# Kernel optimization log

Hardware: AMD Instinct MI355X
Metric: run time of the kernel (lower is better)

Reference implementation:

```python
import jax, jax.numpy as jnp
import numpy as np

B, T, U, D, V = 4, 400, 100, 512, 1024


def setup_inputs() -> dict:
    key = jax.random.key(0)
    k1, k2, k3, k4, k5, k6 = jax.random.split(key, 6)
    return {
        "source_encodings": jax.random.normal(k1, (B, T, D), dtype=jnp.float32),
        "source_lengths": jax.random.randint(k2, (B,), 1, T + 1, dtype=jnp.int32),
        "target_encodings": jax.random.normal(k3, (B, U, D), dtype=jnp.float32),
        "target_lengths": jax.random.randint(k4, (B,), 1, U + 1, dtype=jnp.int32),
        "W": jax.random.normal(k5, (V, D), dtype=jnp.float32) * (1.0 / np.sqrt(D)),
        "b": jax.random.normal(k6, (V,), dtype=jnp.float32) * 0.01,
    }


def reference(source_encodings, source_lengths, target_encodings, target_lengths, W, b):
    # broadcast add: (B,T,1,D) + (B,1,U,D) -> (B,T,U,D)
    joint = source_encodings[:, :, None, :] + target_encodings[:, None, :, :]
    tanh_out = jnp.tanh(joint)
    # linear: (B,T,U,D) @ (D,V) + b -> (B,T,U,V)
    output = jnp.einsum("btud,vd->btuv", tanh_out, W) + b
    return output, source_lengths, target_lengths
```

## Files before the change

### kernel.cpp

```cpp
#include <hip/hip_runtime.h>

#define Bb 4
#define Tt 400
#define Uu 100
#define Dd 512
#define Vv 1024
#define Mtot (Bb * Tt * Uu)
#define OUT_ELEMS ((size_t)Mtot * Vv)
#define NT 8

typedef unsigned short u16;
typedef unsigned int u32;
typedef short bf16x8 __attribute__((ext_vector_type(8)));
typedef float f32x4 __attribute__((ext_vector_type(4)));
typedef u16 u16x4 __attribute__((ext_vector_type(4)));

__device__ __forceinline__ u16 f2bf(float x) {
    union { float f; u32 u; } v; v.f = x;
    u32 r = v.u + 0x7FFFu + ((v.u >> 16) & 1u);
    return (u16)(r >> 16);
}

__device__ __forceinline__ void async16(const void* g, void* l) {
    __builtin_amdgcn_global_load_lds(
        (const __attribute__((address_space(1))) u32*)g,
        (__attribute__((address_space(3))) u32*)l,
        16, 0, 0);
}

__global__ void tanh_fuse(const float* __restrict__ src,
                          const float* __restrict__ tgt,
                          u16* __restrict__ A) {
    int idx = blockIdx.x * 256 + threadIdx.x;
    int d4 = idx & 127;
    int m  = idx >> 7;
    int b  = m / 40000;
    int r  = m - b * 40000;
    int t  = r / 100;
    int u  = r - t * 100;
    const float4 s = ((const float4*)src)[(b * Tt + t) * 128 + d4];
    const float4 g = ((const float4*)tgt)[(b * Uu + u) * 128 + d4];
    u16x4 o;
    o.x = f2bf(tanhf(s.x + g.x));
    o.y = f2bf(tanhf(s.y + g.y));
    o.z = f2bf(tanhf(s.z + g.z));
    o.w = f2bf(tanhf(s.w + g.w));
    ((u16x4*)A)[idx] = o;
}

__global__ void wconv(const float* __restrict__ W, u16* __restrict__ Wb,
                      const int* __restrict__ slen, const int* __restrict__ tlen,
                      float* __restrict__ out) {
    int idx = blockIdx.x * 256 + threadIdx.x;
    float4 w = ((const float4*)W)[idx];
    u16x4 o;
    o.x = f2bf(w.x); o.y = f2bf(w.y); o.z = f2bf(w.z); o.w = f2bf(w.w);
    ((u16x4*)Wb)[idx] = o;
    if (idx < 4)      out[OUT_ELEMS + idx] = (float)slen[idx];
    else if (idx < 8) out[OUT_ELEMS + idx] = (float)tlen[idx - 4];
}


__device__ __forceinline__ void stg2(const u16* g, u16* l, int off0, int loff) {
    async16(g + off0,         l + loff);
    async16(g + off0 + 32768, l + loff + 4096);
}

__global__ __launch_bounds__(512, 2) void gemm8(const u16* __restrict__ A,
                                                const u16* __restrict__ Wb,
                                                const float* __restrict__ bias,
                                                float* __restrict__ out) {
    __shared__ u16 sm[65536];

    const int tid = threadIdx.x;
    const int orig = blockIdx.x;
    const int xcd = orig & 7, loc = orig >> 3;
    const int wg = (xcd < 4 ? xcd * 313 : 1252 + (xcd - 4) * 312) + loc;
    const int bm = wg >> 2;
    const int bn = wg & 3;

    const int lane = tid & 63, wave = tid >> 6;
    const int wm = wave >> 2, wn = wave & 3;
    const int l15 = lane & 15, quad = lane >> 4;
    const int sx = l15 & 7;
    const int c0 = (quad ^ sx) * 8;
    const int c1 = ((4 | quad) ^ sx) * 8;

    const int srow = tid >> 3;
    const int skc  = (tid & 7) ^ (srow & 7);
    const int off0 = srow * 512 + skc * 8;
    const int loff = tid * 8;

    const u16* GA = A  + (size_t)bm * 131072;
    const u16* GB = Wb + (size_t)bn * 131072;

    f32x4 acc[8][4] = {};

    stg2(GA,                 sm,                 off0, loff);
    stg2(GA + 65536,         sm + 8192,          off0, loff);
    stg2(GB,                 sm + 16384,         off0, loff);
    stg2(GB + 65536,         sm + 16384 + 8192,  off0, loff);
    stg2(GA + 64,            sm + 32768,         off0, loff);
    asm volatile("s_waitcnt vmcnt(2)" ::: "memory");
    __builtin_amdgcn_s_barrier();
    __builtin_amdgcn_sched_barrier(0);

    const int bhalf = wn >> 1;
    const int bsub  = (wn & 1) * 4096;

    for (int S = 0; S < NT; ++S) {
        const u16* pA = sm + (S & 1) * 32768 + wm * 8192 + l15 * 64;
        const u16* pB = sm + (S & 1) * 32768 + 16384 + bhalf * 8192 + bsub + l15 * 64;
        u16* nb = sm + ((S + 1) & 1) * 32768;
        u16* cb = sm + (S & 1) * 32768;
        bf16x8 af[4][2], bA[2][2], bB[2][2];

#pragma unroll
        for (int i = 0; i < 4; ++i) {
            af[i][0] = *(const bf16x8*)&pA[i * 1024 + c0];
            af[i][1] = *(const bf16x8*)&pA[i * 1024 + c1];
        }
#pragma unroll
        for (int j = 0; j < 2; ++j) {
            bA[j][0] = *(const bf16x8*)&pB[j * 1024 + c0];
            bA[j][1] = *(const bf16x8*)&pB[j * 1024 + c1];
        }
        if (S + 1 < NT) stg2(GA + 65536 + (S + 1) * 64, nb + 8192, off0, loff);
        __builtin_amdgcn_s_barrier();
        asm volatile("s_waitcnt lgkmcnt(0)" ::: "memory");
        __builtin_amdgcn_sched_barrier(0);
        __builtin_amdgcn_s_setprio(1);
#pragma unroll
        for (int i = 0; i < 4; ++i)
#pragma unroll
            for (int j = 0; j < 2; ++j)
#pragma unroll
                for (int kk = 0; kk < 2; ++kk)
                    acc[i][j] = __builtin_amdgcn_mfma_f32_16x16x32_bf16(
                        af[i][kk], bA[j][kk], acc[i][j], 0, 0, 0);
        __builtin_amdgcn_s_setprio(0);
        __builtin_amdgcn_s_barrier();
        asm volatile("" ::: "memory");

#pragma unroll
        for (int j = 0; j < 2; ++j) {
            bB[j][0] = *(const bf16x8*)&pB[(j + 2) * 1024 + c0];
            bB[j][1] = *(const bf16x8*)&pB[(j + 2) * 1024 + c1];
        }
        if (S + 1 < NT) stg2(GB + (S + 1) * 64, nb + 16384, off0, loff);
        __builtin_amdgcn_s_barrier();
        asm volatile("s_waitcnt lgkmcnt(0)" ::: "memory");
        __builtin_amdgcn_sched_barrier(0);
        __builtin_amdgcn_s_setprio(1);
#pragma unroll
        for (int i = 0; i < 4; ++i)
#pragma unroll
            for (int j = 0; j < 2; ++j)
#pragma unroll
                for (int kk = 0; kk < 2; ++kk)
                    acc[i][j + 2] = __builtin_amdgcn_mfma_f32_16x16x32_bf16(
                        af[i][kk], bB[j][kk], acc[i][j + 2], 0, 0, 0);
        __builtin_amdgcn_s_setprio(0);
        __builtin_amdgcn_s_barrier();
        asm volatile("" ::: "memory");

#pragma unroll
        for (int i = 0; i < 4; ++i) {
            af[i][0] = *(const bf16x8*)&pA[(i + 4) * 1024 + c0];
            af[i][1] = *(const bf16x8*)&pA[(i + 4) * 1024 + c1];
        }
        if (S + 1 < NT) stg2(GB + 65536 + (S + 1) * 64, nb + 16384 + 8192, off0, loff);
        __builtin_amdgcn_s_barrier();
        asm volatile("s_waitcnt lgkmcnt(0)" ::: "memory");
        __builtin_amdgcn_sched_barrier(0);
        __builtin_amdgcn_s_setprio(1);
#pragma unroll
        for (int i = 0; i < 4; ++i)
#pragma unroll
            for (int j = 0; j < 2; ++j)
#pragma unroll
                for (int kk = 0; kk < 2; ++kk)
                    acc[i + 4][j + 2] = __builtin_amdgcn_mfma_f32_16x16x32_bf16(
                        af[i][kk], bB[j][kk], acc[i + 4][j + 2], 0, 0, 0);
        __builtin_amdgcn_s_setprio(0);
        __builtin_amdgcn_s_barrier();
        asm volatile("" ::: "memory");

        if (S + 2 < NT) stg2(GA + (S + 2) * 64, cb, off0, loff);
        __builtin_amdgcn_s_barrier();
        __builtin_amdgcn_s_setprio(1);
#pragma unroll
        for (int i = 0; i < 4; ++i)
#pragma unroll
            for (int j = 0; j < 2; ++j)
#pragma unroll
                for (int kk = 0; kk < 2; ++kk)
                    acc[i + 4][j] = __builtin_amdgcn_mfma_f32_16x16x32_bf16(
                        af[i][kk], bA[j][kk], acc[i + 4][j], 0, 0, 0);
        __builtin_amdgcn_s_setprio(0);
        if (S + 2 < NT)      { asm volatile("s_waitcnt vmcnt(2)" ::: "memory"); }
        else if (S + 1 < NT) { asm volatile("s_waitcnt vmcnt(0)" ::: "memory"); }
        __builtin_amdgcn_s_barrier();
        asm volatile("" ::: "memory");
    }

    const int col0 = bn * 256 + wn * 64 + l15;
    const int rb   = bm * 256 + wm * 128 + quad * 4;
    float bv[4];
#pragma unroll
    for (int j = 0; j < 4; ++j) bv[j] = bias[col0 + j * 16];
#pragma unroll
    for (int i = 0; i < 8; ++i) {
#pragma unroll
        for (int r = 0; r < 4; ++r) {
            float* op = out + (size_t)(rb + i * 16 + r) * 1024 + col0;
#pragma unroll
            for (int j = 0; j < 4; ++j) op[j * 16] = acc[i][j][r] + bv[j];
        }
    }
}

__global__ __launch_bounds__(256) void gemm_inl(const float* __restrict__ src,
                                                const float* __restrict__ tgt,
                                                const float* __restrict__ W,
                                                const float* __restrict__ bias,
                                                float* __restrict__ out) {
    __shared__ u16 lA[128 * 64];
    __shared__ u16 lB[128 * 64];
    const int tid  = threadIdx.x;
    const int bn   = blockIdx.x & 7;
    const int bm   = blockIdx.x >> 3;
    const int lane = tid & 63;
    const int wave = tid >> 6;
    const int wm   = wave >> 1, wn = wave & 1;
    const int l15  = lane & 15, quad = lane >> 4;

    f32x4 acc[4][4] = {};

    const int srow = tid >> 3;
    const int skc  = (tid & 7) * 8;

    const u16* pa = &lA[(wm * 64 + l15) * 64 + quad * 8];
    const u16* pb = &lB[(wn * 64 + l15) * 64 + quad * 8];

    for (int kt = 0; kt < 8; ++kt) {
        const int k0 = kt * 64;
#pragma unroll
        for (int r = 0; r < 4; ++r) {
            const int c   = r * 256 + tid;
            const int row = r * 32 + srow;
            int m = bm * 128 + row;
            int b = m / 40000;
            int rem = m - b * 40000;
            int t = rem / 100;
            int u = rem - t * 100;
            const float* sp = src + (size_t)(b * Tt + t) * 512 + k0 + skc;
            const float* gp = tgt + (size_t)(b * Uu + u) * 512 + k0 + skc;
            float4 s0 = *(const float4*)sp, s1 = *(const float4*)(sp + 4);
            float4 g0 = *(const float4*)gp, g1 = *(const float4*)(gp + 4);
            bf16x8 pk;
            pk[0] = (short)f2bf(tanhf(s0.x + g0.x));
            pk[1] = (short)f2bf(tanhf(s0.y + g0.y));
            pk[2] = (short)f2bf(tanhf(s0.z + g0.z));
            pk[3] = (short)f2bf(tanhf(s0.w + g0.w));
            pk[4] = (short)f2bf(tanhf(s1.x + g1.x));
            pk[5] = (short)f2bf(tanhf(s1.y + g1.y));
            pk[6] = (short)f2bf(tanhf(s1.z + g1.z));
            pk[7] = (short)f2bf(tanhf(s1.w + g1.w));
            *(bf16x8*)&lA[c * 8] = pk;
            const float* wp = W + (size_t)(bn * 128 + row) * 512 + k0 + skc;
            float4 w0 = *(const float4*)wp, w1 = *(const float4*)(wp + 4);
            bf16x8 wk;
            wk[0] = (short)f2bf(w0.x); wk[1] = (short)f2bf(w0.y);
            wk[2] = (short)f2bf(w0.z); wk[3] = (short)f2bf(w0.w);
            wk[4] = (short)f2bf(w1.x); wk[5] = (short)f2bf(w1.y);
            wk[6] = (short)f2bf(w1.z); wk[7] = (short)f2bf(w1.w);
            *(bf16x8*)&lB[c * 8] = wk;
        }
        __syncthreads();
#pragma unroll
        for (int kk = 0; kk < 2; ++kk) {
            bf16x8 af[4], bfr[4];
#pragma unroll
            for (int i = 0; i < 4; ++i)
                af[i] = *(const bf16x8*)&pa[i * 1024 + kk * 32];
#pragma unroll
            for (int j = 0; j < 4; ++j)
                bfr[j] = *(const bf16x8*)&pb[j * 1024 + kk * 32];
#pragma unroll
            for (int i = 0; i < 4; ++i)
#pragma unroll
                for (int j = 0; j < 4; ++j)
                    acc[i][j] = __builtin_amdgcn_mfma_f32_16x16x32_bf16(
                        af[i], bfr[j], acc[i][j], 0, 0, 0);
        }
        __syncthreads();
    }

    const int col0  = bn * 128 + wn * 64 + l15;
    const int rbase = bm * 128 + wm * 64 + quad * 4;
    float bv[4];
#pragma unroll
    for (int j = 0; j < 4; ++j) bv[j] = bias[col0 + j * 16];
#pragma unroll
    for (int i = 0; i < 4; ++i) {
#pragma unroll
        for (int r = 0; r < 4; ++r) {
            float* op = out + (size_t)(rbase + i * 16 + r) * 1024 + col0;
#pragma unroll
            for (int j = 0; j < 4; ++j) op[j * 16] = acc[i][j][r] + bv[j];
        }
    }
}

__global__ void lenout(const int* __restrict__ slen, const int* __restrict__ tlen,
                       float* __restrict__ out) {
    int i = threadIdx.x;
    if (i < 4)      out[OUT_ELEMS + i] = (float)slen[i];
    else if (i < 8) out[OUT_ELEMS + i] = (float)tlen[i - 4];
}

extern "C" void kernel_launch(void* const* d_in, const int* in_sizes, int n_in,
                              void* d_out, int out_size, void* d_ws, size_t ws_size,
                              hipStream_t stream) {
    const float* src  = (const float*)d_in[0];
    const int*   slen = (const int*)d_in[1];
    const float* tgt  = (const float*)d_in[2];
    const int*   tlen = (const int*)d_in[3];
    const float* W    = (const float*)d_in[4];
    const float* bias = (const float*)d_in[5];
    float* out = (float*)d_out;

    const size_t needA = (size_t)Mtot * Dd * 2;
    const size_t needW = (size_t)Vv * Dd * 2;

    if (d_ws != nullptr && ws_size >= needA + needW) {
        u16* Abf = (u16*)d_ws;
        u16* Wbf = (u16*)((char*)d_ws + needA);
        tanh_fuse<<<dim3(80000), dim3(256), 0, stream>>>(src, tgt, Abf);
        wconv<<<dim3(512), dim3(256), 0, stream>>>(W, Wbf, slen, tlen, out);
        gemm8<<<dim3(2500), dim3(512), 0, stream>>>(Abf, Wbf, bias, out);
    } else {
        lenout<<<dim3(1), dim3(64), 0, stream>>>(slen, tlen, out);
        gemm_inl<<<dim3(10000), dim3(256), 0, stream>>>(src, tgt, W, bias, out);
    }
}
```

Measured before the change: 823.2 us.

## Make GEMM persistent over ten tiles and use fast tanh with wider fuse stores

The GEMM becomes a persistent kernel: 250 workgroups each walk 10 output tiles in one continuous 80-step software pipeline. Loads for the next tile are prefetched while the current tile finishes, and each tile's epilogue is written out mid-loop. This is meant to remove the per-tile pipeline fill and drain and the launch tail. The tanh kernel now handles 8 elements per thread and uses an exp-based fast tanh in place of tanhf, cutting ALU work and halving the thread count. Costs: 250 blocks may underfill the CUs (only about one wave of occupancy), the stores in the epilogue stall the pipeline, the fixed XCD-aware tile remapping is dropped, and fast_tanh is slightly less accurate.

```diff
diff --git a/kernel.cpp b/kernel.cpp
--- a/kernel.cpp
+++ b/kernel.cpp
@@ -7,7 +7,7 @@
 #define Vv 1024
 #define Mtot (Bb * Tt * Uu)
 #define OUT_ELEMS ((size_t)Mtot * Vv)
-#define NT 8
+#define NSTEP 80
 
 typedef unsigned short u16;
 typedef unsigned int u32;
@@ -21,6 +21,12 @@
     return (u16)(r >> 16);
 }
 
+__device__ __forceinline__ float fast_tanh(float x) {
+    float cx = fminf(9.0f, fmaxf(-9.0f, x));
+    float e  = __expf(cx + cx);
+    return 1.0f - __fdividef(2.0f, e + 1.0f);
+}
+
 __device__ __forceinline__ void async16(const void* g, void* l) {
     __builtin_amdgcn_global_load_lds(
         (const __attribute__((address_space(1))) u32*)g,
@@ -32,20 +38,26 @@
                           const float* __restrict__ tgt,
                           u16* __restrict__ A) {
     int idx = blockIdx.x * 256 + threadIdx.x;
-    int d4 = idx & 127;
-    int m  = idx >> 7;
+    int d8 = idx & 63;
+    int m  = idx >> 6;
     int b  = m / 40000;
     int r  = m - b * 40000;
     int t  = r / 100;
     int u  = r - t * 100;
-    const float4 s = ((const float4*)src)[(b * Tt + t) * 128 + d4];
-    const float4 g = ((const float4*)tgt)[(b * Uu + u) * 128 + d4];
-    u16x4 o;
-    o.x = f2bf(tanhf(s.x + g.x));
-    o.y = f2bf(tanhf(s.y + g.y));
-    o.z = f2bf(tanhf(s.z + g.z));
-    o.w = f2bf(tanhf(s.w + g.w));
-    ((u16x4*)A)[idx] = o;
+    const float4* sp = (const float4*)src + (size_t)(b * Tt + t) * 128 + d8 * 2;
+    const float4* gp = (const float4*)tgt + (size_t)(b * Uu + u) * 128 + d8 * 2;
+    float4 s0 = sp[0], s1 = sp[1];
+    float4 g0 = gp[0], g1 = gp[1];
+    bf16x8 o;
+    o[0] = (short)f2bf(fast_tanh(s0.x + g0.x));
+    o[1] = (short)f2bf(fast_tanh(s0.y + g0.y));
+    o[2] = (short)f2bf(fast_tanh(s0.z + g0.z));
+    o[3] = (short)f2bf(fast_tanh(s0.w + g0.w));
+    o[4] = (short)f2bf(fast_tanh(s1.x + g1.x));
+    o[5] = (short)f2bf(fast_tanh(s1.y + g1.y));
+    o[6] = (short)f2bf(fast_tanh(s1.z + g1.z));
+    o[7] = (short)f2bf(fast_tanh(s1.w + g1.w));
+    ((bf16x8*)A)[idx] = o;
 }
 
 __global__ void wconv(const float* __restrict__ W, u16* __restrict__ Wb,
@@ -66,18 +78,14 @@
     async16(g + off0 + 32768, l + loff + 4096);
 }
 
-__global__ __launch_bounds__(512, 2) void gemm8(const u16* __restrict__ A,
-                                                const u16* __restrict__ Wb,
-                                                const float* __restrict__ bias,
-                                                float* __restrict__ out) {
+__global__ __launch_bounds__(512, 2) void gemm8p(const u16* __restrict__ A,
+                                                 const u16* __restrict__ Wb,
+                                                 const float* __restrict__ bias,
+                                                 float* __restrict__ out) {
     __shared__ u16 sm[65536];
 
     const int tid = threadIdx.x;
-    const int orig = blockIdx.x;
-    const int xcd = orig & 7, loc = orig >> 3;
-    const int wg = (xcd < 4 ? xcd * 313 : 1252 + (xcd - 4) * 312) + loc;
-    const int bm = wg >> 2;
-    const int bn = wg & 3;
+    const int b0  = blockIdx.x * 10;
 
     const int lane = tid & 63, wave = tid >> 6;
     const int wm = wave >> 2, wn = wave & 3;
@@ -91,28 +99,35 @@
     const int off0 = srow * 512 + skc * 8;
     const int loff = tid * 8;
 
-    const u16* GA = A  + (size_t)bm * 131072;
-    const u16* GB = Wb + (size_t)bn * 131072;
+    const int bhalf = wn >> 1;
+    const int bsub  = (wn & 1) * 4096;
 
     f32x4 acc[8][4] = {};
 
-    stg2(GA,                 sm,                 off0, loff);
-    stg2(GA + 65536,         sm + 8192,          off0, loff);
-    stg2(GB,                 sm + 16384,         off0, loff);
-    stg2(GB + 65536,         sm + 16384 + 8192,  off0, loff);
-    stg2(GA + 64,            sm + 32768,         off0, loff);
+    auto stepA = [&](int x) -> const u16* {
+        int wg = b0 + (x >> 3);
+        return A + (size_t)(wg >> 2) * 131072 + (x & 7) * 64;
+    };
+    auto stepB = [&](int x) -> const u16* {
+        int wg = b0 + (x >> 3);
+        return Wb + (size_t)(wg & 3) * 131072 + (x & 7) * 64;
+    };
+
+    stg2(stepA(0),          sm,                 off0, loff);
+    stg2(stepA(0) + 65536,  sm + 8192,          off0, loff);
+    stg2(stepB(0),          sm + 16384,         off0, loff);
+    stg2(stepB(0) + 65536,  sm + 24576,         off0, loff);
+    stg2(stepA(1),          sm + 32768,         off0, loff);
     asm volatile("s_waitcnt vmcnt(2)" ::: "memory");
     __builtin_amdgcn_s_barrier();
     __builtin_amdgcn_sched_barrier(0);
 
-    const int bhalf = wn >> 1;
-    const int bsub  = (wn & 1) * 4096;
-
-    for (int S = 0; S < NT; ++S) {
-        const u16* pA = sm + (S & 1) * 32768 + wm * 8192 + l15 * 64;
-        const u16* pB = sm + (S & 1) * 32768 + 16384 + bhalf * 8192 + bsub + l15 * 64;
-        u16* nb = sm + ((S + 1) & 1) * 32768;
-        u16* cb = sm + (S & 1) * 32768;
+    for (int g = 0; g < NSTEP; ++g) {
+        const int p = g & 1;
+        const u16* pA = sm + p * 32768 + wm * 8192 + l15 * 64;
+        const u16* pB = sm + p * 32768 + 16384 + bhalf * 8192 + bsub + l15 * 64;
+        u16* nb = sm + (p ^ 1) * 32768;
+        u16* cb = sm + p * 32768;
         bf16x8 af[4][2], bA[2][2], bB[2][2];
 
 #pragma unroll
@@ -125,7 +140,7 @@
             bA[j][0] = *(const bf16x8*)&pB[j * 1024 + c0];
             bA[j][1] = *(const bf16x8*)&pB[j * 1024 + c1];
         }
-        if (S + 1 < NT) stg2(GA + 65536 + (S + 1) * 64, nb + 8192, off0, loff);
+        if (g + 1 < NSTEP) stg2(stepA(g + 1) + 65536, nb + 8192, off0, loff);
         __builtin_amdgcn_s_barrier();
         asm volatile("s_waitcnt lgkmcnt(0)" ::: "memory");
         __builtin_amdgcn_sched_barrier(0);
@@ -147,7 +162,7 @@
             bB[j][0] = *(const bf16x8*)&pB[(j + 2) * 1024 + c0];
             bB[j][1] = *(const bf16x8*)&pB[(j + 2) * 1024 + c1];
         }
-        if (S + 1 < NT) stg2(GB + (S + 1) * 64, nb + 16384, off0, loff);
+        if (g + 1 < NSTEP) stg2(stepB(g + 1), nb + 16384, off0, loff);
         __builtin_amdgcn_s_barrier();
         asm volatile("s_waitcnt lgkmcnt(0)" ::: "memory");
         __builtin_amdgcn_sched_barrier(0);
@@ -169,7 +184,7 @@
             af[i][0] = *(const bf16x8*)&pA[(i + 4) * 1024 + c0];
             af[i][1] = *(const bf16x8*)&pA[(i + 4) * 1024 + c1];
         }
-        if (S + 1 < NT) stg2(GB + 65536 + (S + 1) * 64, nb + 16384 + 8192, off0, loff);
+        if (g + 1 < NSTEP) stg2(stepB(g + 1) + 65536, nb + 24576, off0, loff);
         __builtin_amdgcn_s_barrier();
         asm volatile("s_waitcnt lgkmcnt(0)" ::: "memory");
         __builtin_amdgcn_sched_barrier(0);
@@ -186,7 +201,7 @@
         __builtin_amdgcn_s_barrier();
         asm volatile("" ::: "memory");
 
-        if (S + 2 < NT) stg2(GA + (S + 2) * 64, cb, off0, loff);
+        if (g + 2 < NSTEP) stg2(stepA(g + 2), cb, off0, loff);
         __builtin_amdgcn_s_barrier();
         __builtin_amdgcn_s_setprio(1);
 #pragma unroll
@@ -198,24 +213,33 @@
                     acc[i + 4][j] = __builtin_amdgcn_mfma_f32_16x16x32_bf16(
                         af[i][kk], bA[j][kk], acc[i + 4][j], 0, 0, 0);
         __builtin_amdgcn_s_setprio(0);
-        if (S + 2 < NT)      { asm volatile("s_waitcnt vmcnt(2)" ::: "memory"); }
-        else if (S + 1 < NT) { asm volatile("s_waitcnt vmcnt(0)" ::: "memory"); }
+        if (g + 2 < NSTEP)      { asm volatile("s_waitcnt vmcnt(2)" ::: "memory"); }
+        else                    { asm volatile("s_waitcnt vmcnt(0)" ::: "memory"); }
         __builtin_amdgcn_s_barrier();
         asm volatile("" ::: "memory");
-    }
-
-    const int col0 = bn * 256 + wn * 64 + l15;
-    const int rb   = bm * 256 + wm * 128 + quad * 4;
-    float bv[4];
-#pragma unroll
-    for (int j = 0; j < 4; ++j) bv[j] = bias[col0 + j * 16];
-#pragma unroll
-    for (int i = 0; i < 8; ++i) {
-#pragma unroll
-        for (int r = 0; r < 4; ++r) {
-            float* op = out + (size_t)(rb + i * 16 + r) * 1024 + col0;
-#pragma unroll
-            for (int j = 0; j < 4; ++j) op[j * 16] = acc[i][j][r] + bv[j];
+
+        if ((g & 7) == 7) {
+            const int wg = b0 + (g >> 3);
+            const int bm = wg >> 2, bn = wg & 3;
+            const int col0 = bn * 256 + wn * 64 + l15;
+            const int rb   = bm * 256 + wm * 128 + quad * 4;
+            float bv[4];
+#pragma unroll
+            for (int j = 0; j < 4; ++j) bv[j] = bias[col0 + j * 16];
+#pragma unroll
+            for (int i = 0; i < 8; ++i) {
+#pragma unroll
+                for (int r = 0; r < 4; ++r) {
+                    float* op = out + (size_t)(rb + i * 16 + r) * 1024 + col0;
+#pragma unroll
+                    for (int j = 0; j < 4; ++j) op[j * 16] = acc[i][j][r] + bv[j];
+                }
+            }
+            const f32x4 zz = {0.f, 0.f, 0.f, 0.f};
+#pragma unroll
+            for (int i = 0; i < 8; ++i)
+#pragma unroll
+                for (int j = 0; j < 4; ++j) acc[i][j] = zz;
         }
     }
 }
@@ -259,14 +283,14 @@
             float4 s0 = *(const float4*)sp, s1 = *(const float4*)(sp + 4);
             float4 g0 = *(const float4*)gp, g1 = *(const float4*)(gp + 4);
             bf16x8 pk;
-            pk[0] = (short)f2bf(tanhf(s0.x + g0.x));
-            pk[1] = (short)f2bf(tanhf(s0.y + g0.y));
-            pk[2] = (short)f2bf(tanhf(s0.z + g0.z));
-            pk[3] = (short)f2bf(tanhf(s0.w + g0.w));
-            pk[4] = (short)f2bf(tanhf(s1.x + g1.x));
-            pk[5] = (short)f2bf(tanhf(s1.y + g1.y));
-            pk[6] = (short)f2bf(tanhf(s1.z + g1.z));
-            pk[7] = (short)f2bf(tanhf(s1.w + g1.w));
+            pk[0] = (short)f2bf(fast_tanh(s0.x + g0.x));
+            pk[1] = (short)f2bf(fast_tanh(s0.y + g0.y));
+            pk[2] = (short)f2bf(fast_tanh(s0.z + g0.z));
+            pk[3] = (short)f2bf(fast_tanh(s0.w + g0.w));
+            pk[4] = (short)f2bf(fast_tanh(s1.x + g1.x));
+            pk[5] = (short)f2bf(fast_tanh(s1.y + g1.y));
+            pk[6] = (short)f2bf(fast_tanh(s1.z + g1.z));
+            pk[7] = (short)f2bf(fast_tanh(s1.w + g1.w));
             *(bf16x8*)&lA[c * 8] = pk;
             const float* wp = W + (size_t)(bn * 128 + row) * 512 + k0 + skc;
             float4 w0 = *(const float4*)wp, w1 = *(const float4*)(wp + 4);
@@ -337,9 +361,9 @@
     if (d_ws != nullptr && ws_size >= needA + needW) {
         u16* Abf = (u16*)d_ws;
         u16* Wbf = (u16*)((char*)d_ws + needA);
-        tanh_fuse<<<dim3(80000), dim3(256), 0, stream>>>(src, tgt, Abf);
+        tanh_fuse<<<dim3(40000), dim3(256), 0, stream>>>(src, tgt, Abf);
         wconv<<<dim3(512), dim3(256), 0, stream>>>(W, Wbf, slen, tlen, out);
-        gemm8<<<dim3(2500), dim3(512), 0, stream>>>(Abf, Wbf, bias, out);
+        gemm8p<<<dim3(250), dim3(512), 0, stream>>>(Abf, Wbf, bias, out);
     } else {
         lenout<<<dim3(1), dim3(64), 0, stream>>>(slen, tlen, out);
         gemm_inl<<<dim3(10000), dim3(256), 0, stream>>>(src, tgt, W, bias, out);
```

After: 803.8 us. -2.4%, faster.
